# Optimization experiments

Hardware: AMD Instinct MI355X
Metric: run time of the kernel (lower is better)

Reference implementation:

```python
import jax, jax.numpy as jnp
import numpy as np

N_NODES = 50000
N_FEAT = 128
N_RAND_EDGES = 800000
EPS = 1e-12


def _att_edge_weights(x, row, col, n_node):
    """GNNGuard att_coef: per-edge cosine sim, threshold, zero diagonal,
    row-wise L1 normalize, self-loop weight 1/(deg+1), then exp."""
    # cosine similarity per edge via normalized features (avoids NxN matrix)
    norms = jnp.sqrt(jnp.sum(x * x, axis=1, keepdims=True))
    xn = x / jnp.maximum(norms, EPS)
    sim = jnp.sum(xn[row] * xn[col], axis=1)          # [E]
    sim = jnp.where(sim < 0.1, 0.0, sim)              # threshold
    is_self = (row == col)
    sim = jnp.where(is_self, 0.0, sim)                # remove diagonal (self-sim==1)
    # row-wise L1 normalization (sim >= 0 after threshold)
    rowsum = jax.ops.segment_sum(sim, row, num_segments=n_node)
    rs = rowsum[row]
    sim_norm = jnp.where(rs > 0, sim / jnp.where(rs > 0, rs, 1.0), 0.0)
    # degree = number of nonzero normalized entries per row
    deg = jax.ops.segment_sum((sim_norm != 0).astype(sim.dtype), row,
                              num_segments=n_node)
    lam = 1.0 / (deg + 1.0)                           # self-loop gating weight
    w = jnp.where(is_self, lam[row], sim_norm)
    return jnp.exp(w)


def _gcn_conv(x, row, col, edge_weight, W, b, n_node):
    """GCNConv: h = XW; symmetric-normalized weighted aggregation + bias."""
    h = x @ W                                          # [N, out]
    deg = jax.ops.segment_sum(edge_weight, col, num_segments=n_node)
    dinv = jnp.where(deg > 0, jax.lax.rsqrt(jnp.where(deg > 0, deg, 1.0)), 0.0)
    norm = dinv[row] * edge_weight * dinv[col]         # [E]
    out = jax.ops.segment_sum(norm[:, None] * h[row], col, num_segments=n_node)
    return out + b


def setup_inputs() -> dict:
    key = jax.random.key(0)
    ks = jax.random.split(key, 10)
    x = jax.random.normal(ks[0], (N_NODES, N_FEAT), dtype=jnp.float32)
    # random edges with no self-loops, then append all self-loops
    row = jax.random.randint(ks[1], (N_RAND_EDGES,), 0, N_NODES, dtype=jnp.int32)
    off = jax.random.randint(ks[2], (N_RAND_EDGES,), 1, N_NODES, dtype=jnp.int32)
    col = (row + off) % N_NODES
    loops = jnp.arange(N_NODES, dtype=jnp.int32)
    edge_index = jnp.stack([jnp.concatenate([row, loops]),
                            jnp.concatenate([col, loops])], axis=0)
    s = 1.0 / np.sqrt(N_FEAT)
    W0 = jax.random.normal(ks[3], (N_FEAT, 128), dtype=jnp.float32) * s
    b0 = jnp.zeros((128,), dtype=jnp.float32)
    W1 = jax.random.normal(ks[4], (128, 128), dtype=jnp.float32) * s
    b1 = jnp.zeros((128,), dtype=jnp.float32)
    W2 = jax.random.normal(ks[5], (128, 40), dtype=jnp.float32) * s
    b2 = jnp.zeros((40,), dtype=jnp.float32)
    gate = jax.random.uniform(ks[6], (2,), dtype=jnp.float32)
    return {"x": x, "gate": gate, "W0": W0, "b0": b0, "W1": W1, "b1": b1,
            "W2": W2, "b2": b2, "edge_index": edge_index}


def reference(x, gate, W0, b0, W1, b1, W2, b2, edge_index):
    n = x.shape[0]
    row, col = edge_index[0], edge_index[1]
    Ws = [(W0, b0), (W1, b1), (W2, b2)]
    # layer 0: attention adj from raw features (kept as base adj for gating)
    adj_vals = _att_edge_weights(x, row, col, n)
    h = _gcn_conv(x, row, col, adj_vals, W0, b0, n)
    h = jax.nn.relu(h)
    for i in range(1, 3):
        e_new = _att_edge_weights(h, row, col, n)
        g = gate[i - 1]
        w = g * adj_vals + (1.0 - g) * e_new
        h = _gcn_conv(h, row, col, w, Ws[i][0], Ws[i][1], n)
        if i != 2:
            h = jax.nn.relu(h)
    return jax.nn.log_softmax(h, axis=1)
```

## Files before the change

### kernel.cpp

```cpp
#include <hip/hip_runtime.h>
#include <hip/hip_bf16.h>
#include <math.h>

#define F 128

typedef __attribute__((ext_vector_type(8))) short bf16x8;
typedef __attribute__((ext_vector_type(4))) float f32x4;

__global__ void k_normalize(const float* __restrict__ x, float* __restrict__ xn,
                            __hip_bfloat16* __restrict__ xnb, int N) {
  int wid = (blockIdx.x * blockDim.x + threadIdx.x) >> 6;
  int lane = threadIdx.x & 63;
  if (wid >= N) return;
  const float2* src = (const float2*)(x + (size_t)wid * F);
  float2 v = src[lane];
  float ss = v.x * v.x + v.y * v.y;
#pragma unroll
  for (int m = 32; m >= 1; m >>= 1) ss += __shfl_xor(ss, m);
  float inv = 1.0f / fmaxf(sqrtf(ss), 1e-12f);
  float2 o; o.x = v.x * inv; o.y = v.y * inv;
  ((float2*)(xn + (size_t)wid * F))[lane] = o;
  __hip_bfloat162 ob;
  ob.x = __float2bfloat16(o.x); ob.y = __float2bfloat16(o.y);
  ((__hip_bfloat162*)(xnb + (size_t)wid * F))[lane] = ob;
}

__global__ __launch_bounds__(256) void k_lhist(
    const int* __restrict__ keys, const int* __restrict__ perm,
    int* __restrict__ ghist, int* __restrict__ keyout, int nchunk, int E) {
  __shared__ int lh[256];
  int t = threadIdx.x, chunk = blockIdx.x;
  lh[t] = 0;
  __syncthreads();
  int base = chunk * 2048;
#pragma unroll
  for (int k = 0; k < 8; ++k) {
    int i = base + k * 256 + t;
    if (i < E) {
      int key = perm ? keys[perm[i]] : keys[i];
      if (keyout) keyout[i] = key;
      atomicAdd(&lh[key >> 8], 1);
    }
  }
  __syncthreads();
  ghist[t * nchunk + chunk] = lh[t];
}

__global__ void k_scan1(const int* __restrict__ cnt, int* __restrict__ partial,
                        int* __restrict__ bsum, int M) {
  __shared__ int sm[256];
  int t = threadIdx.x;
  int i = blockIdx.x * 256 + t;
  int val = (i < M) ? cnt[i] : 0;
  sm[t] = val;
  __syncthreads();
  for (int off = 1; off < 256; off <<= 1) {
    int v = (t >= off) ? sm[t - off] : 0;
    __syncthreads();
    sm[t] += v;
    __syncthreads();
  }
  if (i < M) partial[i] = sm[t] - val;
  if (t == 255) bsum[blockIdx.x] = sm[255];
}

__global__ void k_scan2(const int* __restrict__ bsum, int* __restrict__ boffs, int nb) {
  __shared__ int sm[256];
  int t = threadIdx.x;
  int carry = 0;
  for (int base = 0; base < nb; base += 256) {
    int idx = base + t;
    int val = (idx < nb) ? bsum[idx] : 0;
    sm[t] = val;
    __syncthreads();
    for (int off = 1; off < 256; off <<= 1) {
      int v = (t >= off) ? sm[t - off] : 0;
      __syncthreads();
      sm[t] += v;
      __syncthreads();
    }
    if (idx < nb) boffs[idx] = sm[t] - val + carry;
    carry += sm[255];
    __syncthreads();
  }
}

__global__ __launch_bounds__(256) void k_bucketize(
    const int* __restrict__ keys, const int* __restrict__ perm,
    const int* __restrict__ partial, const int* __restrict__ boffs,
    int* __restrict__ ebuck, int nchunk, int E) {
  __shared__ int lcur[256];
  int t = threadIdx.x, chunk = blockIdx.x;
  int idx = t * nchunk + chunk;
  lcur[t] = partial[idx] + boffs[idx >> 8];
  __syncthreads();
  int base = chunk * 2048;
#pragma unroll
  for (int k = 0; k < 8; ++k) {
    int i = base + k * 256 + t;
    if (i < E) {
      int key = perm ? keys[perm[i]] : keys[i];
      int pos = atomicAdd(&lcur[key >> 8], 1);
      ebuck[pos] = (i << 8) | (key & 255);
    }
  }
}

__global__ __launch_bounds__(256) void k_final_row(
    const int* __restrict__ ebuck, const int* __restrict__ partial,
    const int* __restrict__ boffs, int* __restrict__ perm_r,
    int* __restrict__ offs_r, int nchunk, int N, int E) {
  __shared__ int lh[256], sm[256], lscan[256];
  int t = threadIdx.x, b = blockIdx.x;
  int i0 = b * nchunk;
  int start = partial[i0] + boffs[i0 >> 8];
  int i1 = i0 + nchunk;
  int end = (b < 255) ? partial[i1] + boffs[i1 >> 8] : E;
  lh[t] = 0;
  __syncthreads();
  for (int p = start + t; p < end; p += 256) atomicAdd(&lh[ebuck[p] & 255], 1);
  __syncthreads();
  int val = lh[t];
  sm[t] = val;
  __syncthreads();
  for (int off = 1; off < 256; off <<= 1) {
    int v = (t >= off) ? sm[t - off] : 0;
    __syncthreads();
    sm[t] += v;
    __syncthreads();
  }
  lscan[t] = sm[t] - val;
  int node = b * 256 + t;
  if (node < N) offs_r[node] = start + lscan[t];
  if (b == 0 && t == 0) offs_r[N] = E;
  lh[t] = 0;
  __syncthreads();
  for (int p = start + t; p < end; p += 256) {
    int v = ebuck[p];
    int low = v & 255;
    int rk = atomicAdd(&lh[low], 1);
    perm_r[start + lscan[low] + rk] = v >> 8;
  }
}

__global__ __launch_bounds__(256) void k_final_col(
    const int* __restrict__ ebuck, const int* __restrict__ perm_r,
    const int* __restrict__ row, const int* __restrict__ partial,
    const int* __restrict__ boffs, int2* __restrict__ pstat,
    int* __restrict__ offs_c, int nchunk, int N, int E) {
  __shared__ int lh[256], sm[256], lscan[256];
  int t = threadIdx.x, b = blockIdx.x;
  int i0 = b * nchunk;
  int start = partial[i0] + boffs[i0 >> 8];
  int i1 = i0 + nchunk;
  int end = (b < 255) ? partial[i1] + boffs[i1 >> 8] : E;
  lh[t] = 0;
  __syncthreads();
  for (int p = start + t; p < end; p += 256) atomicAdd(&lh[ebuck[p] & 255], 1);
  __syncthreads();
  int val = lh[t];
  sm[t] = val;
  __syncthreads();
  for (int off = 1; off < 256; off <<= 1) {
    int v = (t >= off) ? sm[t - off] : 0;
    __syncthreads();
    sm[t] += v;
    __syncthreads();
  }
  lscan[t] = sm[t] - val;
  int node = b * 256 + t;
  if (node < N) offs_c[node] = start + lscan[t];
  if (b == 0 && t == 0) offs_c[N] = E;
  lh[t] = 0;
  __syncthreads();
  for (int p = start + t; p < end; p += 256) {
    int v = ebuck[p];
    int low = v & 255;
    int rp = v >> 8;
    int e = perm_r[rp];
    int rk = atomicAdd(&lh[low], 1);
    int2 rec; rec.x = row[e]; rec.y = rp;
    pstat[start + lscan[low] + rk] = rec;
  }
}

__global__ __launch_bounds__(256) void k_simw(
    const float* __restrict__ xn, const __hip_bfloat16* __restrict__ xnb,
    const int* __restrict__ colof_r, const int* __restrict__ offs_r,
    float* __restrict__ adjr, float* __restrict__ wgr,
    const float* __restrict__ gate, int layer, int N) {
  int w = threadIdx.x >> 6;
  int l = threadIdx.x & 63;
  int r = blockIdx.x * 4 + w;
  __shared__ float sims[4][320];
  __shared__ int scol[4][320];
  if (r >= N) return;
  int p0 = offs_r[r], p1 = offs_r[r + 1];
  int ne = p1 - p0;
  int quad = l >> 4;
  int m = l & 15;
  int qoff = quad * 8;
  const __hip_bfloat16* xr = xnb + (size_t)r * F;
  bf16x8 b0 = *(const bf16x8*)(xr + 0 * 32 + qoff);
  bf16x8 b1 = *(const bf16x8*)(xr + 1 * 32 + qoff);
  bf16x8 b2 = *(const bf16x8*)(xr + 2 * 32 + qoff);
  bf16x8 b3 = *(const bf16x8*)(xr + 3 * 32 + qoff);
  for (int tb = 0; tb < ne; tb += 16) {
    int ii = tb + m; if (ii > ne - 1) ii = ne - 1;
    int cm = colof_r[p0 + ii];
    if (quad == 0 && tb + m < ne) scol[w][tb + m] = cm;
    const __hip_bfloat16* xc = xnb + (size_t)cm * F;
    bf16x8 a0 = *(const bf16x8*)(xc + 0 * 32 + qoff);
    bf16x8 a1 = *(const bf16x8*)(xc + 1 * 32 + qoff);
    bf16x8 a2 = *(const bf16x8*)(xc + 2 * 32 + qoff);
    bf16x8 a3 = *(const bf16x8*)(xc + 3 * 32 + qoff);
    f32x4 acc = {0.f, 0.f, 0.f, 0.f};
    acc = __builtin_amdgcn_mfma_f32_16x16x32_bf16(a0, b0, acc, 0, 0, 0);
    acc = __builtin_amdgcn_mfma_f32_16x16x32_bf16(a1, b1, acc, 0, 0, 0);
    acc = __builtin_amdgcn_mfma_f32_16x16x32_bf16(a2, b2, acc, 0, 0, 0);
    acc = __builtin_amdgcn_mfma_f32_16x16x32_bf16(a3, b3, acc, 0, 0, 0);
    if (m == 0) {
#pragma unroll
      for (int reg = 0; reg < 4; ++reg) {
        int i = tb + quad * 4 + reg;
        if (i < ne) sims[w][i] = acc[reg];
      }
    }
  }
  float vsum = 0.f; int cn = 0;
  for (int base = 0; base < ne; base += 64) {
    int i = base + l;
    bool have = i < ne;
    float s = have ? sims[w][i] : 0.f;
    int c = have ? scol[w][i] : r;
    bool self = (c == r);
    bool flag = have && !self && fabsf(s - 0.1f) < 0.01f;
    unsigned long long mask = __ballot(flag);
    while (mask) {
      int src = __ffsll(mask) - 1;
      mask &= mask - 1;
      int cc = __shfl(c, src);
      float2 ar = ((const float2*)(xn + (size_t)r * F))[l];
      float2 bc = ((const float2*)(xn + (size_t)cc * F))[l];
      float d = ar.x * bc.x + ar.y * bc.y;
#pragma unroll
      for (int mm = 32; mm >= 1; mm >>= 1) d += __shfl_xor(d, mm);
      if (l == src) s = d;
    }
    if (self || s < 0.1f) s = 0.f;
    if (have) sims[w][i] = s;
    vsum += s;
    cn += (s > 0.f) ? 1 : 0;
  }
#pragma unroll
  for (int mm = 32; mm >= 1; mm >>= 1) {
    vsum += __shfl_xor(vsum, mm);
    cn += __shfl_xor(cn, mm);
  }
  float rs = vsum;
  float lam = 1.0f / (float)(cn + 1);
  float gg = (layer > 0) ? gate[layer - 1] : 0.f;
  for (int i = l; i < ne; i += 64) {
    int c = scol[w][i];
    float s = sims[w][i];
    float sn = (rs > 0.f) ? s / rs : 0.f;
    float wv = (c == r) ? lam : sn;
    wv = expf(wv);
    float wc;
    if (layer == 0) { adjr[p0 + i] = wv; wc = wv; }
    else { wc = gg * adjr[p0 + i] + (1.f - gg) * wv; }
    wgr[p0 + i] = wc;
  }
}

__global__ __launch_bounds__(256) void k_colw(
    const int2* __restrict__ pstat, const float* __restrict__ wgr,
    const int* __restrict__ offs_c, float* __restrict__ dinv, int N) {
  int c = blockIdx.x * 256 + threadIdx.x;
  if (c >= N) return;
  int p0 = offs_c[c], p1 = offs_c[c + 1];
  float s = 0.f;
  int p = p0;
  for (; p + 4 <= p1; p += 4) {
    int2 a = pstat[p], b = pstat[p + 1], d = pstat[p + 2], e = pstat[p + 3];
    s += wgr[a.y] + wgr[b.y] + wgr[d.y] + wgr[e.y];
  }
  for (; p < p1; ++p) s += wgr[pstat[p].y];
  dinv[c] = (s > 0.f) ? rsqrtf(s) : 0.f;
}

__global__ __launch_bounds__(256) void k_nrm(
    const int2* __restrict__ pstat, const float* __restrict__ wgr,
    const float* __restrict__ dinv, const int* __restrict__ offs_c,
    int2* __restrict__ packed, int N) {
  int c = blockIdx.x * 256 + threadIdx.x;
  if (c >= N) return;
  int p0 = offs_c[c], p1 = offs_c[c + 1];
  float dic = dinv[c];
  for (int p = p0; p < p1; ++p) {
    int2 s = pstat[p];
    float nrm = dinv[s.x] * wgr[s.y] * dic;
    int2 rec; rec.x = s.x; rec.y = __float_as_int(nrm);
    packed[p] = rec;
  }
}

__global__ __launch_bounds__(256) void k_gemm128(const void* __restrict__ Av,
                                                 int a_bf16,
                                                 const float* __restrict__ W,
                                                 __hip_bfloat16* __restrict__ out, int M) {
  __shared__ float As[128][36];
  int t = threadIdx.x;
  int n0 = blockIdx.x * 32;
  for (int i = t; i < 32 * 128; i += 256) {
    int nn = i >> 7, kk = i & 127;
    int gn = n0 + nn;
    float v = 0.f;
    if (gn < M) {
      if (a_bf16) v = __bfloat162float(((const __hip_bfloat16*)Av)[(size_t)gn * 128 + kk]);
      else v = ((const float*)Av)[(size_t)gn * 128 + kk];
    }
    As[kk][nn] = v;
  }
  __syncthreads();
  int nb = (t >> 6) * 8;
  int j2 = (t & 63) * 2;
  float acc[8][2] = {};
  for (int k = 0; k < 128; ++k) {
    float4 a01 = *(const float4*)&As[k][nb];
    float4 a23 = *(const float4*)&As[k][nb + 4];
    float2 wv = *(const float2*)&W[k * 128 + j2];
    acc[0][0] += a01.x * wv.x; acc[0][1] += a01.x * wv.y;
    acc[1][0] += a01.y * wv.x; acc[1][1] += a01.y * wv.y;
    acc[2][0] += a01.z * wv.x; acc[2][1] += a01.z * wv.y;
    acc[3][0] += a01.w * wv.x; acc[3][1] += a01.w * wv.y;
    acc[4][0] += a23.x * wv.x; acc[4][1] += a23.x * wv.y;
    acc[5][0] += a23.y * wv.x; acc[5][1] += a23.y * wv.y;
    acc[6][0] += a23.z * wv.x; acc[6][1] += a23.z * wv.y;
    acc[7][0] += a23.w * wv.x; acc[7][1] += a23.w * wv.y;
  }
  __hip_bfloat162* o2 = (__hip_bfloat162*)out;
#pragma unroll
  for (int i = 0; i < 8; ++i) {
    int gn = n0 + nb + i;
    if (gn < M) {
      __hip_bfloat162 o;
      o.x = __float2bfloat16(acc[i][0]); o.y = __float2bfloat16(acc[i][1]);
      o2[(size_t)gn * 64 + (j2 >> 1)] = o;
    }
  }
}

__global__ __launch_bounds__(320) void k_gemm40(const __hip_bfloat16* __restrict__ A,
                                                const float* __restrict__ W,
                                                __hip_bfloat16* __restrict__ out,
                                                int M, int C) {
  __shared__ float As[128][68];
  int t = threadIdx.x;
  int n0 = blockIdx.x * 64;
  for (int i = t; i < 64 * 128; i += 320) {
    int nn = i >> 7, kk = i & 127;
    int gn = n0 + nn;
    As[kk][nn] = (gn < M) ? __bfloat162float(A[(size_t)gn * 128 + kk]) : 0.f;
  }
  __syncthreads();
  int gq = t / 40;
  int jc = t - gq * 40;
  int nb = gq * 8;
  float acc[8] = {};
  for (int k = 0; k < 128; ++k) {
    float4 a01 = *(const float4*)&As[k][nb];
    float4 a23 = *(const float4*)&As[k][nb + 4];
    float wv = W[k * C + jc];
    acc[0] += a01.x * wv; acc[1] += a01.y * wv; acc[2] += a01.z * wv; acc[3] += a01.w * wv;
    acc[4] += a23.x * wv; acc[5] += a23.y * wv; acc[6] += a23.z * wv; acc[7] += a23.w * wv;
  }
#pragma unroll
  for (int i = 0; i < 8; ++i) {
    int gn = n0 + nb + i;
    if (gn < M) out[(size_t)gn * C + jc] = __float2bfloat16(acc[i]);
  }
}

__global__ __launch_bounds__(256) void k_agg_norm(
    const __hip_bfloat162* __restrict__ hWb, const int2* __restrict__ packed,
    const int* __restrict__ offs_c, const float* __restrict__ bias,
    __hip_bfloat16* __restrict__ outb, float* __restrict__ xn,
    __hip_bfloat16* __restrict__ xnb, int N) {
  int w = threadIdx.x >> 6;
  int t = threadIdx.x & 63;
  int c = blockIdx.x * 4 + w;
  if (c >= N) return;
  int p0 = offs_c[c], p1 = offs_c[c + 1];
  float acc0 = bias[2 * t], acc1 = bias[2 * t + 1];
  int p = p0;
  for (; p + 8 <= p1; p += 8) {
    int2 s[8];
    __hip_bfloat162 h[8];
#pragma unroll
    for (int k = 0; k < 8; ++k) s[k] = packed[p + k];
#pragma unroll
    for (int k = 0; k < 8; ++k) h[k] = hWb[(size_t)s[k].x * 64 + t];
#pragma unroll
    for (int k = 0; k < 8; ++k) {
      float n = __int_as_float(s[k].y);
      acc0 += n * __bfloat162float(h[k].x);
      acc1 += n * __bfloat162float(h[k].y);
    }
  }
  for (; p + 4 <= p1; p += 4) {
    int2 s0 = packed[p], s1 = packed[p + 1], s2 = packed[p + 2], s3 = packed[p + 3];
    __hip_bfloat162 h0 = hWb[(size_t)s0.x * 64 + t];
    __hip_bfloat162 h1 = hWb[(size_t)s1.x * 64 + t];
    __hip_bfloat162 h2 = hWb[(size_t)s2.x * 64 + t];
    __hip_bfloat162 h3 = hWb[(size_t)s3.x * 64 + t];
    float n0 = __int_as_float(s0.y), n1 = __int_as_float(s1.y);
    float n2 = __int_as_float(s2.y), n3 = __int_as_float(s3.y);
    acc0 += n0 * __bfloat162float(h0.x) + n1 * __bfloat162float(h1.x)
          + n2 * __bfloat162float(h2.x) + n3 * __bfloat162float(h3.x);
    acc1 += n0 * __bfloat162float(h0.y) + n1 * __bfloat162float(h1.y)
          + n2 * __bfloat162float(h2.y) + n3 * __bfloat162float(h3.y);
  }
  for (; p < p1; ++p) {
    int2 s0 = packed[p];
    __hip_bfloat162 h0 = hWb[(size_t)s0.x * 64 + t];
    float n0 = __int_as_float(s0.y);
    acc0 += n0 * __bfloat162float(h0.x);
    acc1 += n0 * __bfloat162float(h0.y);
  }
  acc0 = fmaxf(acc0, 0.f); acc1 = fmaxf(acc1, 0.f);
  __hip_bfloat162 oh;
  oh.x = __float2bfloat16(acc0); oh.y = __float2bfloat16(acc1);
  ((__hip_bfloat162*)outb)[(size_t)c * 64 + t] = oh;
  float ss = acc0 * acc0 + acc1 * acc1;
#pragma unroll
  for (int m = 32; m >= 1; m >>= 1) ss += __shfl_xor(ss, m);
  float inv = 1.0f / fmaxf(sqrtf(ss), 1e-12f);
  float2 on; on.x = acc0 * inv; on.y = acc1 * inv;
  ((float2*)xn)[(size_t)c * 64 + t] = on;
  __hip_bfloat162 ob;
  ob.x = __float2bfloat16(on.x); ob.y = __float2bfloat16(on.y);
  ((__hip_bfloat162*)xnb)[(size_t)c * 64 + t] = ob;
}

__global__ __launch_bounds__(256) void k_agg40_lsm(
    const __hip_bfloat16* __restrict__ hW, const int2* __restrict__ packed,
    const int* __restrict__ offs_c, const float* __restrict__ bias,
    float* __restrict__ out, int C, int N) {
  int w = threadIdx.x >> 6;
  int j = threadIdx.x & 63;
  int c = blockIdx.x * 4 + w;
  if (c >= N) return;
  int p0 = offs_c[c], p1 = offs_c[c + 1];
  bool act = j < C;
  int jj = act ? j : 0;
  float acc = act ? bias[jj] : 0.f;
  int p = p0;
  for (; p + 4 <= p1; p += 4) {
    int2 s0 = packed[p], s1 = packed[p + 1], s2 = packed[p + 2], s3 = packed[p + 3];
    float h0 = __bfloat162float(hW[(size_t)s0.x * C + jj]);
    float h1 = __bfloat162float(hW[(size_t)s1.x * C + jj]);
    float h2 = __bfloat162float(hW[(size_t)s2.x * C + jj]);
    float h3 = __bfloat162float(hW[(size_t)s3.x * C + jj]);
    acc += __int_as_float(s0.y) * h0 + __int_as_float(s1.y) * h1
         + __int_as_float(s2.y) * h2 + __int_as_float(s3.y) * h3;
  }
  for (; p < p1; ++p) {
    int2 s0 = packed[p];
    acc += __int_as_float(s0.y) * __bfloat162float(hW[(size_t)s0.x * C + jj]);
  }
  if (!act) acc = 0.f;
  float v = act ? acc : -3.0e38f;
#pragma unroll
  for (int m = 32; m >= 1; m >>= 1) v = fmaxf(v, __shfl_xor(v, m));
  float ex = act ? expf(acc - v) : 0.f;
#pragma unroll
  for (int m = 32; m >= 1; m >>= 1) ex += __shfl_xor(ex, m);
  if (act) out[(size_t)c * C + j] = acc - v - logf(ex);
}

extern "C" void kernel_launch(void* const* d_in, const int* in_sizes, int n_in,
                              void* d_out, int out_size, void* d_ws, size_t ws_size,
                              hipStream_t stream) {
  const float* x    = (const float*)d_in[0];
  const float* gate = (const float*)d_in[1];
  const float* W0   = (const float*)d_in[2];
  const float* b0   = (const float*)d_in[3];
  const float* W1   = (const float*)d_in[4];
  const float* b1   = (const float*)d_in[5];
  const float* W2   = (const float*)d_in[6];
  const float* b2   = (const float*)d_in[7];
  const int* eidx   = (const int*)d_in[8];
  int N = in_sizes[0] / 128;
  int E = in_sizes[8] / 2;
  int C = in_sizes[7];
  const int* row = eidx;
  const int* col = eidx + E;

  char* ws = (char*)d_ws;
  size_t off = 0;
  auto alloc = [&](size_t bytes) {
    char* p = ws + off;
    off += (bytes + 255) & ~(size_t)255;
    return p;
  };
  float* xn     = (float*)alloc((size_t)N * 128 * 4);
  __hip_bfloat16* xnb  = (__hip_bfloat16*)alloc((size_t)N * 128 * 2);
  __hip_bfloat16* bufC = (__hip_bfloat16*)alloc((size_t)N * 128 * 2);
  __hip_bfloat16* hWb  = (__hip_bfloat16*)alloc((size_t)N * 128 * 2);
  float* adjr   = (float*)alloc((size_t)E * 4);
  float* wgr    = (float*)alloc((size_t)E * 4);
  int*   perm_r = (int*)alloc((size_t)E * 4);
  int2*  pstat  = (int2*)alloc((size_t)E * 8);
  int2*  packed = (int2*)alloc((size_t)E * 8);
  int*   colof_r= (int*)alloc((size_t)E * 4);
  int*   ebuck  = (int*)alloc((size_t)E * 4);
  int*   offs_c = (int*)alloc((size_t)(N + 1) * 4);
  int*   offs_r = (int*)alloc((size_t)(N + 1) * 4);
  float* dinv   = (float*)alloc((size_t)N * 4);

  int NCHUNK = (E + 2047) / 2048;
  int M      = 256 * NCHUNK;
  int*   ghist  = (int*)alloc((size_t)M * 4);
  int*   partial= (int*)alloc((size_t)M * 4);
  int*   bsum   = (int*)alloc((size_t)NCHUNK * 4);
  int*   boffs  = (int*)alloc((size_t)NCHUNK * 4);

  int NBUK = (N + 255) / 256;
  int nb1  = (N + 255) / 256;
  int nw4  = (N + 3) / 4;

  k_lhist<<<NCHUNK, 256, 0, stream>>>(row, nullptr, ghist, nullptr, NCHUNK, E);
  k_scan1<<<NCHUNK, 256, 0, stream>>>(ghist, partial, bsum, M);
  k_scan2<<<1, 256, 0, stream>>>(bsum, boffs, NCHUNK);
  k_bucketize<<<NCHUNK, 256, 0, stream>>>(row, nullptr, partial, boffs, ebuck, NCHUNK, E);
  k_final_row<<<NBUK, 256, 0, stream>>>(ebuck, partial, boffs, perm_r, offs_r,
                                        NCHUNK, N, E);
  k_lhist<<<NCHUNK, 256, 0, stream>>>(col, perm_r, ghist, colof_r, NCHUNK, E);
  k_scan1<<<NCHUNK, 256, 0, stream>>>(ghist, partial, bsum, M);
  k_scan2<<<1, 256, 0, stream>>>(bsum, boffs, NCHUNK);
  k_bucketize<<<NCHUNK, 256, 0, stream>>>(col, perm_r, partial, boffs, ebuck, NCHUNK, E);
  k_final_col<<<NBUK, 256, 0, stream>>>(ebuck, perm_r, row, partial, boffs, pstat,
                                        offs_c, NCHUNK, N, E);

  for (int layer = 0; layer < 3; ++layer) {
    if (layer == 0) k_normalize<<<(N + 3) / 4, 256, 0, stream>>>(x, xn, xnb, N);
    k_simw<<<nw4, 256, 0, stream>>>(xn, xnb, colof_r, offs_r, adjr, wgr,
                                    gate, layer, N);
    k_colw<<<nb1, 256, 0, stream>>>(pstat, wgr, offs_c, dinv, N);
    k_nrm<<<nb1, 256, 0, stream>>>(pstat, wgr, dinv, offs_c, packed, N);
    if (layer < 2) {
      const float* W = (layer == 0) ? W0 : W1;
      const float* b = (layer == 0) ? b0 : b1;
      if (layer == 0)
        k_gemm128<<<(N + 31) / 32, 256, 0, stream>>>((const void*)x, 0, W, hWb, N);
      else
        k_gemm128<<<(N + 31) / 32, 256, 0, stream>>>((const void*)bufC, 1, W, hWb, N);
      k_agg_norm<<<nw4, 256, 0, stream>>>((const __hip_bfloat162*)hWb, packed, offs_c,
                                          b, bufC, xn, xnb, N);
    } else {
      k_gemm40<<<(N + 63) / 64, 320, 0, stream>>>(bufC, W2, hWb, N, C);
      k_agg40_lsm<<<nw4, 256, 0, stream>>>(hWb, packed, offs_c, b2, (float*)d_out, C, N);
    }
  }
}
```

Before: 614.3 us.

## Merge similarity and GEMM launches; compute edge norms inline during aggregation

The similarity/edge-weight kernel and the 128-wide feature GEMM are now launched as one grid, with blocks dispatched by block index to either task. This lets the two independent stages run concurrently and saves a launch. The separate k_nrm pass that materialized packed normalized weights is removed. The aggregation kernels now gather dinv and wgr per edge and compute the norm inline, trading an extra write/read pass for more random gathers in the aggregation loop.

```diff
diff --git a/kernel.cpp b/kernel.cpp
--- a/kernel.cpp
+++ b/kernel.cpp
@@ -184,92 +184,138 @@
   }
 }
 
-__global__ __launch_bounds__(256) void k_simw(
+__global__ __launch_bounds__(256) void k_simw_gemm(
     const float* __restrict__ xn, const __hip_bfloat16* __restrict__ xnb,
     const int* __restrict__ colof_r, const int* __restrict__ offs_r,
     float* __restrict__ adjr, float* __restrict__ wgr,
-    const float* __restrict__ gate, int layer, int N) {
-  int w = threadIdx.x >> 6;
-  int l = threadIdx.x & 63;
-  int r = blockIdx.x * 4 + w;
-  __shared__ float sims[4][320];
-  __shared__ int scol[4][320];
-  if (r >= N) return;
-  int p0 = offs_r[r], p1 = offs_r[r + 1];
-  int ne = p1 - p0;
-  int quad = l >> 4;
-  int m = l & 15;
-  int qoff = quad * 8;
-  const __hip_bfloat16* xr = xnb + (size_t)r * F;
-  bf16x8 b0 = *(const bf16x8*)(xr + 0 * 32 + qoff);
-  bf16x8 b1 = *(const bf16x8*)(xr + 1 * 32 + qoff);
-  bf16x8 b2 = *(const bf16x8*)(xr + 2 * 32 + qoff);
-  bf16x8 b3 = *(const bf16x8*)(xr + 3 * 32 + qoff);
-  for (int tb = 0; tb < ne; tb += 16) {
-    int ii = tb + m; if (ii > ne - 1) ii = ne - 1;
-    int cm = colof_r[p0 + ii];
-    if (quad == 0 && tb + m < ne) scol[w][tb + m] = cm;
-    const __hip_bfloat16* xc = xnb + (size_t)cm * F;
-    bf16x8 a0 = *(const bf16x8*)(xc + 0 * 32 + qoff);
-    bf16x8 a1 = *(const bf16x8*)(xc + 1 * 32 + qoff);
-    bf16x8 a2 = *(const bf16x8*)(xc + 2 * 32 + qoff);
-    bf16x8 a3 = *(const bf16x8*)(xc + 3 * 32 + qoff);
-    f32x4 acc = {0.f, 0.f, 0.f, 0.f};
-    acc = __builtin_amdgcn_mfma_f32_16x16x32_bf16(a0, b0, acc, 0, 0, 0);
-    acc = __builtin_amdgcn_mfma_f32_16x16x32_bf16(a1, b1, acc, 0, 0, 0);
-    acc = __builtin_amdgcn_mfma_f32_16x16x32_bf16(a2, b2, acc, 0, 0, 0);
-    acc = __builtin_amdgcn_mfma_f32_16x16x32_bf16(a3, b3, acc, 0, 0, 0);
-    if (m == 0) {
-#pragma unroll
-      for (int reg = 0; reg < 4; ++reg) {
-        int i = tb + quad * 4 + reg;
-        if (i < ne) sims[w][i] = acc[reg];
+    const float* __restrict__ gate, int layer, int N, int nw4,
+    const void* __restrict__ Av, int a_bf16, const float* __restrict__ W,
+    __hip_bfloat16* __restrict__ gout, int doGemm) {
+  __shared__ __align__(16) char smem[18432];
+  if ((int)blockIdx.x < nw4) {
+    float (*sims)[320] = (float(*)[320])smem;
+    int (*scol)[320] = (int(*)[320])(smem + 5120);
+    int w = threadIdx.x >> 6;
+    int l = threadIdx.x & 63;
+    int r = blockIdx.x * 4 + w;
+    if (r >= N) return;
+    int p0 = offs_r[r], p1 = offs_r[r + 1];
+    int ne = p1 - p0;
+    int quad = l >> 4;
+    int m = l & 15;
+    int qoff = quad * 8;
+    const __hip_bfloat16* xr = xnb + (size_t)r * F;
+    bf16x8 b0 = *(const bf16x8*)(xr + 0 * 32 + qoff);
+    bf16x8 b1 = *(const bf16x8*)(xr + 1 * 32 + qoff);
+    bf16x8 b2 = *(const bf16x8*)(xr + 2 * 32 + qoff);
+    bf16x8 b3 = *(const bf16x8*)(xr + 3 * 32 + qoff);
+    for (int tb = 0; tb < ne; tb += 16) {
+      int ii = tb + m; if (ii > ne - 1) ii = ne - 1;
+      int cm = colof_r[p0 + ii];
+      if (quad == 0 && tb + m < ne) scol[w][tb + m] = cm;
+      const __hip_bfloat16* xc = xnb + (size_t)cm * F;
+      bf16x8 a0 = *(const bf16x8*)(xc + 0 * 32 + qoff);
+      bf16x8 a1 = *(const bf16x8*)(xc + 1 * 32 + qoff);
+      bf16x8 a2 = *(const bf16x8*)(xc + 2 * 32 + qoff);
+      bf16x8 a3 = *(const bf16x8*)(xc + 3 * 32 + qoff);
+      f32x4 acc = {0.f, 0.f, 0.f, 0.f};
+      acc = __builtin_amdgcn_mfma_f32_16x16x32_bf16(a0, b0, acc, 0, 0, 0);
+      acc = __builtin_amdgcn_mfma_f32_16x16x32_bf16(a1, b1, acc, 0, 0, 0);
+      acc = __builtin_amdgcn_mfma_f32_16x16x32_bf16(a2, b2, acc, 0, 0, 0);
+      acc = __builtin_amdgcn_mfma_f32_16x16x32_bf16(a3, b3, acc, 0, 0, 0);
+      if (m == 0) {
+#pragma unroll
+        for (int reg = 0; reg < 4; ++reg) {
+          int i = tb + quad * 4 + reg;
+          if (i < ne) sims[w][i] = acc[reg];
+        }
       }
     }
-  }
-  float vsum = 0.f; int cn = 0;
-  for (int base = 0; base < ne; base += 64) {
-    int i = base + l;
-    bool have = i < ne;
-    float s = have ? sims[w][i] : 0.f;
-    int c = have ? scol[w][i] : r;
-    bool self = (c == r);
-    bool flag = have && !self && fabsf(s - 0.1f) < 0.01f;
-    unsigned long long mask = __ballot(flag);
-    while (mask) {
-      int src = __ffsll(mask) - 1;
-      mask &= mask - 1;
-      int cc = __shfl(c, src);
-      float2 ar = ((const float2*)(xn + (size_t)r * F))[l];
-      float2 bc = ((const float2*)(xn + (size_t)cc * F))[l];
-      float d = ar.x * bc.x + ar.y * bc.y;
-#pragma unroll
-      for (int mm = 32; mm >= 1; mm >>= 1) d += __shfl_xor(d, mm);
-      if (l == src) s = d;
-    }
-    if (self || s < 0.1f) s = 0.f;
-    if (have) sims[w][i] = s;
-    vsum += s;
-    cn += (s > 0.f) ? 1 : 0;
-  }
-#pragma unroll
-  for (int mm = 32; mm >= 1; mm >>= 1) {
-    vsum += __shfl_xor(vsum, mm);
-    cn += __shfl_xor(cn, mm);
-  }
-  float rs = vsum;
-  float lam = 1.0f / (float)(cn + 1);
-  float gg = (layer > 0) ? gate[layer - 1] : 0.f;
-  for (int i = l; i < ne; i += 64) {
-    int c = scol[w][i];
-    float s = sims[w][i];
-    float sn = (rs > 0.f) ? s / rs : 0.f;
-    float wv = (c == r) ? lam : sn;
-    wv = expf(wv);
-    float wc;
-    if (layer == 0) { adjr[p0 + i] = wv; wc = wv; }
-    else { wc = gg * adjr[p0 + i] + (1.f - gg) * wv; }
-    wgr[p0 + i] = wc;
+    float vsum = 0.f; int cn = 0;
+    for (int base = 0; base < ne; base += 64) {
+      int i = base + l;
+      bool have = i < ne;
+      float s = have ? sims[w][i] : 0.f;
+      int c = have ? scol[w][i] : r;
+      bool self = (c == r);
+      bool flag = have && !self && fabsf(s - 0.1f) < 0.01f;
+      unsigned long long mask = __ballot(flag);
+      while (mask) {
+        int src = __ffsll(mask) - 1;
+        mask &= mask - 1;
+        int cc = __shfl(c, src);
+        float2 ar = ((const float2*)(xn + (size_t)r * F))[l];
+        float2 bc = ((const float2*)(xn + (size_t)cc * F))[l];
+        float d = ar.x * bc.x + ar.y * bc.y;
+#pragma unroll
+        for (int mm = 32; mm >= 1; mm >>= 1) d += __shfl_xor(d, mm);
+        if (l == src) s = d;
+      }
+      if (self || s < 0.1f) s = 0.f;
+      if (have) sims[w][i] = s;
+      vsum += s;
+      cn += (s > 0.f) ? 1 : 0;
+    }
+#pragma unroll
+    for (int mm = 32; mm >= 1; mm >>= 1) {
+      vsum += __shfl_xor(vsum, mm);
+      cn += __shfl_xor(cn, mm);
+    }
+    float rs = vsum;
+    float lam = 1.0f / (float)(cn + 1);
+    float gg = (layer > 0) ? gate[layer - 1] : 0.f;
+    for (int i = l; i < ne; i += 64) {
+      int c = scol[w][i];
+      float s = sims[w][i];
+      float sn = (rs > 0.f) ? s / rs : 0.f;
+      float wv = (c == r) ? lam : sn;
+      wv = expf(wv);
+      float wc;
+      if (layer == 0) { adjr[p0 + i] = wv; wc = wv; }
+      else { wc = gg * adjr[p0 + i] + (1.f - gg) * wv; }
+      wgr[p0 + i] = wc;
+    }
+  } else if (doGemm) {
+    float (*As)[36] = (float(*)[36])smem;
+    int t = threadIdx.x;
+    int n0 = ((int)blockIdx.x - nw4) * 32;
+    for (int i = t; i < 32 * 128; i += 256) {
+      int nn = i >> 7, kk = i & 127;
+      int gn = n0 + nn;
+      float v = 0.f;
+      if (gn < N) {
+        if (a_bf16) v = __bfloat162float(((const __hip_bfloat16*)Av)[(size_t)gn * 128 + kk]);
+        else v = ((const float*)Av)[(size_t)gn * 128 + kk];
+      }
+      As[kk][nn] = v;
+    }
+    __syncthreads();
+    int nb = (t >> 6) * 8;
+    int j2 = (t & 63) * 2;
+    float acc[8][2] = {};
+    for (int k = 0; k < 128; ++k) {
+      float4 a01 = *(const float4*)&As[k][nb];
+      float4 a23 = *(const float4*)&As[k][nb + 4];
+      float2 wv = *(const float2*)&W[k * 128 + j2];
+      acc[0][0] += a01.x * wv.x; acc[0][1] += a01.x * wv.y;
+      acc[1][0] += a01.y * wv.x; acc[1][1] += a01.y * wv.y;
+      acc[2][0] += a01.z * wv.x; acc[2][1] += a01.z * wv.y;
+      acc[3][0] += a01.w * wv.x; acc[3][1] += a01.w * wv.y;
+      acc[4][0] += a23.x * wv.x; acc[4][1] += a23.x * wv.y;
+      acc[5][0] += a23.y * wv.x; acc[5][1] += a23.y * wv.y;
+      acc[6][0] += a23.z * wv.x; acc[6][1] += a23.z * wv.y;
+      acc[7][0] += a23.w * wv.x; acc[7][1] += a23.w * wv.y;
+    }
+    __hip_bfloat162* o2 = (__hip_bfloat162*)gout;
+#pragma unroll
+    for (int i = 0; i < 8; ++i) {
+      int gn = n0 + nb + i;
+      if (gn < N) {
+        __hip_bfloat162 o;
+        o.x = __float2bfloat16(acc[i][0]); o.y = __float2bfloat16(acc[i][1]);
+        o2[(size_t)gn * 64 + (j2 >> 1)] = o;
+      }
+    }
   }
 }
 
@@ -289,68 +335,6 @@
   dinv[c] = (s > 0.f) ? rsqrtf(s) : 0.f;
 }
 
-__global__ __launch_bounds__(256) void k_nrm(
-    const int2* __restrict__ pstat, const float* __restrict__ wgr,
-    const float* __restrict__ dinv, const int* __restrict__ offs_c,
-    int2* __restrict__ packed, int N) {
-  int c = blockIdx.x * 256 + threadIdx.x;
-  if (c >= N) return;
-  int p0 = offs_c[c], p1 = offs_c[c + 1];
-  float dic = dinv[c];
-  for (int p = p0; p < p1; ++p) {
-    int2 s = pstat[p];
-    float nrm = dinv[s.x] * wgr[s.y] * dic;
-    int2 rec; rec.x = s.x; rec.y = __float_as_int(nrm);
-    packed[p] = rec;
-  }
-}
-
-__global__ __launch_bounds__(256) void k_gemm128(const void* __restrict__ Av,
-                                                 int a_bf16,
-                                                 const float* __restrict__ W,
-                                                 __hip_bfloat16* __restrict__ out, int M) {
-  __shared__ float As[128][36];
-  int t = threadIdx.x;
-  int n0 = blockIdx.x * 32;
-  for (int i = t; i < 32 * 128; i += 256) {
-    int nn = i >> 7, kk = i & 127;
-    int gn = n0 + nn;
-    float v = 0.f;
-    if (gn < M) {
-      if (a_bf16) v = __bfloat162float(((const __hip_bfloat16*)Av)[(size_t)gn * 128 + kk]);
-      else v = ((const float*)Av)[(size_t)gn * 128 + kk];
-    }
-    As[kk][nn] = v;
-  }
-  __syncthreads();
-  int nb = (t >> 6) * 8;
-  int j2 = (t & 63) * 2;
-  float acc[8][2] = {};
-  for (int k = 0; k < 128; ++k) {
-    float4 a01 = *(const float4*)&As[k][nb];
-    float4 a23 = *(const float4*)&As[k][nb + 4];
-    float2 wv = *(const float2*)&W[k * 128 + j2];
-    acc[0][0] += a01.x * wv.x; acc[0][1] += a01.x * wv.y;
-    acc[1][0] += a01.y * wv.x; acc[1][1] += a01.y * wv.y;
-    acc[2][0] += a01.z * wv.x; acc[2][1] += a01.z * wv.y;
-    acc[3][0] += a01.w * wv.x; acc[3][1] += a01.w * wv.y;
-    acc[4][0] += a23.x * wv.x; acc[4][1] += a23.x * wv.y;
-    acc[5][0] += a23.y * wv.x; acc[5][1] += a23.y * wv.y;
-    acc[6][0] += a23.z * wv.x; acc[6][1] += a23.z * wv.y;
-    acc[7][0] += a23.w * wv.x; acc[7][1] += a23.w * wv.y;
-  }
-  __hip_bfloat162* o2 = (__hip_bfloat162*)out;
-#pragma unroll
-  for (int i = 0; i < 8; ++i) {
-    int gn = n0 + nb + i;
-    if (gn < M) {
-      __hip_bfloat162 o;
-      o.x = __float2bfloat16(acc[i][0]); o.y = __float2bfloat16(acc[i][1]);
-      o2[(size_t)gn * 64 + (j2 >> 1)] = o;
-    }
-  }
-}
-
 __global__ __launch_bounds__(320) void k_gemm40(const __hip_bfloat16* __restrict__ A,
                                                 const float* __restrict__ W,
                                                 __hip_bfloat16* __restrict__ out,
@@ -383,7 +367,8 @@
 }
 
 __global__ __launch_bounds__(256) void k_agg_norm(
-    const __hip_bfloat162* __restrict__ hWb, const int2* __restrict__ packed,
+    const __hip_bfloat162* __restrict__ hWb, const int2* __restrict__ pstat,
+    const float* __restrict__ wgr, const float* __restrict__ dinv,
     const int* __restrict__ offs_c, const float* __restrict__ bias,
     __hip_bfloat16* __restrict__ outb, float* __restrict__ xn,
     __hip_bfloat16* __restrict__ xnb, int N) {
@@ -392,39 +377,29 @@
   int c = blockIdx.x * 4 + w;
   if (c >= N) return;
   int p0 = offs_c[c], p1 = offs_c[c + 1];
+  float dic = dinv[c];
   float acc0 = bias[2 * t], acc1 = bias[2 * t + 1];
   int p = p0;
   for (; p + 8 <= p1; p += 8) {
     int2 s[8];
     __hip_bfloat162 h[8];
-#pragma unroll
-    for (int k = 0; k < 8; ++k) s[k] = packed[p + k];
+    float nw[8];
+#pragma unroll
+    for (int k = 0; k < 8; ++k) s[k] = pstat[p + k];
 #pragma unroll
     for (int k = 0; k < 8; ++k) h[k] = hWb[(size_t)s[k].x * 64 + t];
 #pragma unroll
+    for (int k = 0; k < 8; ++k) nw[k] = dinv[s[k].x] * wgr[s[k].y] * dic;
+#pragma unroll
     for (int k = 0; k < 8; ++k) {
-      float n = __int_as_float(s[k].y);
-      acc0 += n * __bfloat162float(h[k].x);
-      acc1 += n * __bfloat162float(h[k].y);
-    }
-  }
-  for (; p + 4 <= p1; p += 4) {
-    int2 s0 = packed[p], s1 = packed[p + 1], s2 = packed[p + 2], s3 = packed[p + 3];
+      acc0 += nw[k] * __bfloat162float(h[k].x);
+      acc1 += nw[k] * __bfloat162float(h[k].y);
+    }
+  }
+  for (; p < p1; ++p) {
+    int2 s0 = pstat[p];
     __hip_bfloat162 h0 = hWb[(size_t)s0.x * 64 + t];
-    __hip_bfloat162 h1 = hWb[(size_t)s1.x * 64 + t];
-    __hip_bfloat162 h2 = hWb[(size_t)s2.x * 64 + t];
-    __hip_bfloat162 h3 = hWb[(size_t)s3.x * 64 + t];
-    float n0 = __int_as_float(s0.y), n1 = __int_as_float(s1.y);
-    float n2 = __int_as_float(s2.y), n3 = __int_as_float(s3.y);
-    acc0 += n0 * __bfloat162float(h0.x) + n1 * __bfloat162float(h1.x)
-          + n2 * __bfloat162float(h2.x) + n3 * __bfloat162float(h3.x);
-    acc1 += n0 * __bfloat162float(h0.y) + n1 * __bfloat162float(h1.y)
-          + n2 * __bfloat162float(h2.y) + n3 * __bfloat162float(h3.y);
-  }
-  for (; p < p1; ++p) {
-    int2 s0 = packed[p];
-    __hip_bfloat162 h0 = hWb[(size_t)s0.x * 64 + t];
-    float n0 = __int_as_float(s0.y);
+    float n0 = dinv[s0.x] * wgr[s0.y] * dic;
     acc0 += n0 * __bfloat162float(h0.x);
     acc1 += n0 * __bfloat162float(h0.y);
   }
@@ -444,7 +419,8 @@
 }
 
 __global__ __launch_bounds__(256) void k_agg40_lsm(
-    const __hip_bfloat16* __restrict__ hW, const int2* __restrict__ packed,
+    const __hip_bfloat16* __restrict__ hW, const int2* __restrict__ pstat,
+    const float* __restrict__ wgr, const float* __restrict__ dinv,
     const int* __restrict__ offs_c, const float* __restrict__ bias,
     float* __restrict__ out, int C, int N) {
   int w = threadIdx.x >> 6;
@@ -452,22 +428,26 @@
   int c = blockIdx.x * 4 + w;
   if (c >= N) return;
   int p0 = offs_c[c], p1 = offs_c[c + 1];
+  float dic = dinv[c];
   bool act = j < C;
   int jj = act ? j : 0;
   float acc = act ? bias[jj] : 0.f;
   int p = p0;
   for (; p + 4 <= p1; p += 4) {
-    int2 s0 = packed[p], s1 = packed[p + 1], s2 = packed[p + 2], s3 = packed[p + 3];
+    int2 s0 = pstat[p], s1 = pstat[p + 1], s2 = pstat[p + 2], s3 = pstat[p + 3];
     float h0 = __bfloat162float(hW[(size_t)s0.x * C + jj]);
     float h1 = __bfloat162float(hW[(size_t)s1.x * C + jj]);
     float h2 = __bfloat162float(hW[(size_t)s2.x * C + jj]);
     float h3 = __bfloat162float(hW[(size_t)s3.x * C + jj]);
-    acc += __int_as_float(s0.y) * h0 + __int_as_float(s1.y) * h1
-         + __int_as_float(s2.y) * h2 + __int_as_float(s3.y) * h3;
+    acc += dinv[s0.x] * wgr[s0.y] * dic * h0
+         + dinv[s1.x] * wgr[s1.y] * dic * h1
+         + dinv[s2.x] * wgr[s2.y] * dic * h2
+         + dinv[s3.x] * wgr[s3.y] * dic * h3;
   }
   for (; p < p1; ++p) {
-    int2 s0 = packed[p];
-    acc += __int_as_float(s0.y) * __bfloat162float(hW[(size_t)s0.x * C + jj]);
+    int2 s0 = pstat[p];
+    acc += dinv[s0.x] * wgr[s0.y] * dic
+         * __bfloat162float(hW[(size_t)s0.x * C + jj]);
   }
   if (!act) acc = 0.f;
   float v = act ? acc : -3.0e38f;
@@ -512,7 +492,6 @@
   float* wgr    = (float*)alloc((size_t)E * 4);
   int*   perm_r = (int*)alloc((size_t)E * 4);
   int2*  pstat  = (int2*)alloc((size_t)E * 8);
-  int2*  packed = (int2*)alloc((size_t)E * 8);
   int*   colof_r= (int*)alloc((size_t)E * 4);
   int*   ebuck  = (int*)alloc((size_t)E * 4);
   int*   offs_c = (int*)alloc((size_t)(N + 1) * 4);
@@ -529,6 +508,7 @@
   int NBUK = (N + 255) / 256;
   int nb1  = (N + 255) / 256;
   int nw4  = (N + 3) / 4;
+  int gb128 = (N + 31) / 32;
 
   k_lhist<<<NCHUNK, 256, 0, stream>>>(row, nullptr, ghist, nullptr, NCHUNK, E);
   k_scan1<<<NCHUNK, 256, 0, stream>>>(ghist, partial, bsum, M);
@@ -545,22 +525,25 @@
 
   for (int layer = 0; layer < 3; ++layer) {
     if (layer == 0) k_normalize<<<(N + 3) / 4, 256, 0, stream>>>(x, xn, xnb, N);
-    k_simw<<<nw4, 256, 0, stream>>>(xn, xnb, colof_r, offs_r, adjr, wgr,
-                                    gate, layer, N);
-    k_colw<<<nb1, 256, 0, stream>>>(pstat, wgr, offs_c, dinv, N);
-    k_nrm<<<nb1, 256, 0, stream>>>(pstat, wgr, dinv, offs_c, packed, N);
     if (layer < 2) {
       const float* W = (layer == 0) ? W0 : W1;
       const float* b = (layer == 0) ? b0 : b1;
-      if (layer == 0)
-        k_gemm128<<<(N + 31) / 32, 256, 0, stream>>>((const void*)x, 0, W, hWb, N);
-      else
-        k_gemm128<<<(N + 31) / 32, 256, 0, stream>>>((const void*)bufC, 1, W, hWb, N);
-      k_agg_norm<<<nw4, 256, 0, stream>>>((const __hip_bfloat162*)hWb, packed, offs_c,
-                                          b, bufC, xn, xnb, N);
+      const void* Av = (layer == 0) ? (const void*)x : (const void*)bufC;
+      int abf = (layer == 0) ? 0 : 1;
+      k_simw_gemm<<<nw4 + gb128, 256, 0, stream>>>(xn, xnb, colof_r, offs_r, adjr, wgr,
+                                                   gate, layer, N, nw4,
+                                                   Av, abf, W, hWb, 1);
+      k_colw<<<nb1, 256, 0, stream>>>(pstat, wgr, offs_c, dinv, N);
+      k_agg_norm<<<nw4, 256, 0, stream>>>((const __hip_bfloat162*)hWb, pstat, wgr, dinv,
+                                          offs_c, b, bufC, xn, xnb, N);
     } else {
+      k_simw_gemm<<<nw4, 256, 0, stream>>>(xn, xnb, colof_r, offs_r, adjr, wgr,
+                                           gate, layer, N, nw4,
+                                           nullptr, 0, nullptr, nullptr, 0);
+      k_colw<<<nb1, 256, 0, stream>>>(pstat, wgr, offs_c, dinv, N);
       k_gemm40<<<(N + 63) / 64, 320, 0, stream>>>(bufC, W2, hWb, N, C);
-      k_agg40_lsm<<<nw4, 256, 0, stream>>>(hWb, packed, offs_c, b2, (float*)d_out, C, N);
-    }
-  }
-}
+      k_agg40_lsm<<<nw4, 256, 0, stream>>>(hWb, pstat, wgr, dinv, offs_c, b2,
+                                           (float*)d_out, C, N);
+    }
+  }
+}
```

After: 590.1 us. 1.04x faster.
